# Kernel optimization log

Measured on AMD Instinct MI355X. Metric: run time of the kernel, lower is better.

## Reference

```python
import jax, jax.numpy as jnp
import numpy as np

F = 128   # flattened observation features
H = 64    # MLP/LSTM hidden size (hardcoded in module)
A = 15    # number of discrete actions
T = 128   # rollout length (timesteps)
B = 2048  # number of parallel envs (batch)


def setup_inputs() -> dict:
    key = jax.random.key(0)
    ks = jax.random.split(key, 12)
    n = lambda k, sh, s=1.0: jax.random.normal(k, sh, jnp.float32) * s
    return {
        "x": n(ks[0], (T * B, F)),
        "done": (jax.random.uniform(ks[1], (T * B,)) < 0.05).astype(jnp.float32),
        "h0": n(ks[2], (1, B, H)),
        "c0": n(ks[3], (1, B, H)),
        # MLP encoder params (Linear stores y = x @ W + b here, W: [in, out])
        "W1": n(ks[4], (F, H), 0.1), "b1": jnp.zeros((H,), jnp.float32),
        "W2": n(ks[5], (H, H), 0.1), "b2": jnp.zeros((H,), jnp.float32),
        # LSTM params, PyTorch layout: weight_ih [4H, H_in], gate order i,f,g,o
        "Wih": n(ks[6], (4 * H, H), 0.1), "bih": jnp.zeros((4 * H,), jnp.float32),
        "Whh": n(ks[7], (4 * H, H), 0.1), "bhh": jnp.zeros((4 * H,), jnp.float32),
        # actor / critic heads
        "Wa": n(ks[8], (H, A), 0.01), "ba": jnp.zeros((A,), jnp.float32),
        "Wc": n(ks[9], (H, 1), 1.0), "bc": jnp.zeros((1,), jnp.float32),
    }


def reference(x, done, h0, c0, W1, b1, W2, b2, Wih, bih, Whh, bhh, Wa, ba, Wc, bc):
    Bsz, Hh = h0.shape[1], h0.shape[2]
    # MLP encoder: Linear -> Tanh -> Linear -> Tanh
    y = jnp.tanh(x @ W1 + b1)
    y = jnp.tanh(y @ W2 + b2)                 # [T*B, H]
    y = y.reshape(-1, Bsz, Hh)                # [T, B, H]
    d = done.reshape(-1, Bsz)                 # [T, B]

    def step(carry, td):
        h, c = carry
        yt, dt = td
        m = (1.0 - dt)[:, None]               # done-mask hidden reset
        h = h * m
        c = c * m
        g = yt @ Wih.T + bih + h @ Whh.T + bhh  # [B, 4H]
        i, f, gg, o = jnp.split(g, 4, axis=-1)
        c = jax.nn.sigmoid(f) * c + jax.nn.sigmoid(i) * jnp.tanh(gg)
        h = jax.nn.sigmoid(o) * jnp.tanh(c)
        return (h, c), h

    (hT, cT), outs = jax.lax.scan(step, (h0[0], c0[0]), (y, d))
    z = outs.reshape(-1, Hh)                  # [T*B, H]
    logits = z @ Wa + ba                      # Categorical logits
    vf = z @ Wc + bc
    return logits, vf, hT[None], cT[None]
```

## Files before the change

### kernel.cpp

```cpp
#include <hip/hip_runtime.h>
#include <hip/hip_bf16.h>
#include <stdint.h>

typedef __bf16  bf16x8 __attribute__((ext_vector_type(8)));
typedef short   s16x8  __attribute__((ext_vector_type(8)));
typedef int     i32x4  __attribute__((ext_vector_type(4)));
typedef float   f32x4  __attribute__((ext_vector_type(4)));

union Frag { s16x8 s; bf16x8 b; i32x4 i; };

static __device__ __forceinline__ short f2bf(float f) {
    union { float f; unsigned u; } v; v.f = f;
    unsigned r = (v.u + 0x7FFFu + ((v.u >> 16) & 1u)) >> 16;
    return (short)r;
}
static __device__ __forceinline__ float bf2f(short s) {
    union { unsigned u; float f; } v; v.u = ((unsigned)(unsigned short)s) << 16;
    return v.f;
}
static __device__ __forceinline__ float fast_rcp(float x) { return __builtin_amdgcn_rcpf(x); }
static __device__ __forceinline__ float sigm(float x) { return fast_rcp(1.0f + __expf(-x)); }
static __device__ __forceinline__ float tanh_fast(float x) {
    float e = __expf(-2.0f * x);
    return (1.0f - e) * fast_rcp(1.0f + e);
}
static __device__ __forceinline__ f32x4 mfma16(bf16x8 a, bf16x8 b, f32x4 c) {
    return __builtin_amdgcn_mfma_f32_16x16x32_bf16(a, b, c, 0, 0, 0);
}

static __device__ __forceinline__ void block_sync_lds() {
    asm volatile("s_waitcnt lgkmcnt(0)\n\ts_barrier" ::: "memory");
}

#define GLDS(gp, lp) __builtin_amdgcn_global_load_lds( \
    (const __attribute__((address_space(1))) void*)(gp), \
    (__attribute__((address_space(3))) void*)(lp), 16, 0, 0)

#define TT 128
#define BB 2048
#define HH 64
#define FF 128
#define AA 15
#define CH 8
#define LOGITS_OFF 0
#define VF_OFF   3932160
#define HT_OFF   4194304
#define CT_OFF   4325376


__global__ __launch_bounds__(256) void enc_kernel(
    const float* __restrict__ x, const float* __restrict__ W1, const float* __restrict__ b1,
    const float* __restrict__ W2, const float* __restrict__ b2, short* __restrict__ y_sw)
{
    __shared__ short w1t[64][136];
    __shared__ short w2t[64][72];
    __shared__ short c1buf[4][16][72];
    __shared__ short ybuf[4][16][72];

    const int tid  = threadIdx.x;
    const int lane = tid & 63;
    const int w    = tid >> 6;
    const int c    = lane & 15;
    const int q    = lane >> 4;

    for (int i = tid; i < 128*64; i += 256) { int k = i >> 6, n = i & 63; w1t[n][k] = f2bf(W1[i]); }
    for (int i = tid; i < 64*64;  i += 256) { int k = i >> 6, n = i & 63; w2t[n][k] = f2bf(W2[i]); }

    float b1v[4], b2v[4];
#pragma unroll
    for (int ct = 0; ct < 4; ++ct) { b1v[ct] = b1[16*ct + c]; b2v[ct] = b2[16*ct + c]; }
    __syncthreads();

    for (int it = 0; it < 4; ++it) {
        const int wt = it*4096 + blockIdx.x*4 + w;
        const int r0 = wt * 16;
        Frag af[4];
#pragma unroll
        for (int kf = 0; kf < 4; ++kf) {
            const float* xp = x + (size_t)(r0 + c)*FF + 32*kf + 8*q;
            f32x4 x0 = *(const f32x4*)xp;
            f32x4 x1 = *(const f32x4*)(xp + 4);
#pragma unroll
            for (int jj = 0; jj < 4; ++jj) { af[kf].s[jj] = f2bf(x0[jj]); af[kf].s[4+jj] = f2bf(x1[jj]); }
        }
        f32x4 acc[4];
#pragma unroll
        for (int ct = 0; ct < 4; ++ct) acc[ct] = (f32x4){b1v[ct], b1v[ct], b1v[ct], b1v[ct]};
#pragma unroll
        for (int kf = 0; kf < 4; ++kf)
#pragma unroll
            for (int ct = 0; ct < 4; ++ct) {
                Frag bf; bf.s = *(const s16x8*)&w1t[16*ct + c][32*kf + 8*q];
                acc[ct] = mfma16(af[kf].b, bf.b, acc[ct]);
            }
#pragma unroll
        for (int ct = 0; ct < 4; ++ct)
#pragma unroll
            for (int i = 0; i < 4; ++i)
                c1buf[w][4*q + i][16*ct + c] = f2bf(tanh_fast(acc[ct][i]));
        Frag a2[2];
#pragma unroll
        for (int kf = 0; kf < 2; ++kf) a2[kf].s = *(const s16x8*)&c1buf[w][c][32*kf + 8*q];
        f32x4 acc2[4];
#pragma unroll
        for (int ct = 0; ct < 4; ++ct) acc2[ct] = (f32x4){b2v[ct], b2v[ct], b2v[ct], b2v[ct]};
#pragma unroll
        for (int kf = 0; kf < 2; ++kf)
#pragma unroll
            for (int ct = 0; ct < 4; ++ct) {
                Frag bf; bf.s = *(const s16x8*)&w2t[16*ct + c][32*kf + 8*q];
                acc2[ct] = mfma16(a2[kf].b, bf.b, acc2[ct]);
            }
#pragma unroll
        for (int ct = 0; ct < 4; ++ct)
#pragma unroll
            for (int i = 0; i < 4; ++i)
                ybuf[w][4*q + i][16*ct + c] = f2bf(tanh_fast(acc2[ct][i]));
        {
            const int kf2 = lane >> 5;
            const int c8  = (lane >> 2) & 7;
            const int qq  = lane & 3;
#pragma unroll
            for (int g = 0; g < 2; ++g) {
                s16x8 yv = *(const s16x8*)&ybuf[w][c8 + 8*g][32*kf2 + 8*qq];
                *(s16x8*)(y_sw + ((size_t)(wt >> 7)*256 + (size_t)(wt & 127)*2 + g)*512 + lane*8) = yv;
            }
        }
    }
}

__global__ __launch_bounds__(512, 1) void scan_kernel(
    const short* __restrict__ y_sw, const float* __restrict__ done,
    const float* __restrict__ h0, const float* __restrict__ c0,
    const float* __restrict__ Wih, const float* __restrict__ bih,
    const float* __restrict__ Whh, const float* __restrict__ bhh,
    const float* __restrict__ Wa, const float* __restrict__ ba,
    const float* __restrict__ Wc, const float* __restrict__ bc,
    float* __restrict__ out_logits, float* __restrict__ out_vf,
    float* __restrict__ hT_out, float* __restrict__ cT_out)
{
    __shared__ short ybuf[2][CH][512];
    __shared__ float gybuf[2][4][4][128];
    __shared__ float obuf[2][CH][8][16];
    __shared__ short zbuf[2][8][72];
    __shared__ short hbuf[2][8][72];
    __shared__ float dbuf[TT+1][8];

    const int tid  = threadIdx.x;
    const int lane = tid & 63;
    const int w    = tid >> 6;
    const int c    = lane & 15;
    const int q    = lane >> 4;
    const int blk  = blockIdx.x;
    const int b0   = blk * 8;
    const bool crit = (w < 4);
    const int hw   = w - 4;
    const int r0   = 4*(q & 1) + 2*(q >> 1);

    Frag  wf[4][2];
    float biasv[4];
    Frag  hwf[2];
    float hbv = 0.f;
    float cst0 = 0.f, cst1 = 0.f;

    if (crit) {
        const int jcol = 16*w + c;
#pragma unroll
        for (int a = 0; a < 4; ++a) {
            const int col = 64*a + jcol;
#pragma unroll
            for (int kf = 0; kf < 2; ++kf) {
                const float* wp = Whh + (size_t)col*HH + 32*kf + 8*q;
                f32x4 w0 = *(const f32x4*)wp;
                f32x4 w1 = *(const f32x4*)(wp + 4);
#pragma unroll
                for (int jj = 0; jj < 4; ++jj) { wf[a][kf].s[jj] = f2bf(w0[jj]); wf[a][kf].s[4+jj] = f2bf(w1[jj]); }
            }
        }
    } else {
        const int jcolh = 16*hw + c;
#pragma unroll
        for (int a = 0; a < 4; ++a) {
            const int col = 64*a + jcolh;
            biasv[a] = bih[col] + bhh[col];
#pragma unroll
            for (int kf = 0; kf < 2; ++kf) {
                const float* wp = Wih + (size_t)col*HH + 32*kf + 8*q;
                f32x4 w0 = *(const f32x4*)wp;
                f32x4 w1 = *(const f32x4*)(wp + 4);
#pragma unroll
                for (int jj = 0; jj < 4; ++jj) { wf[a][kf].s[jj] = f2bf(w0[jj]); wf[a][kf].s[4+jj] = f2bf(w1[jj]); }
            }
        }
#pragma unroll
        for (int kf = 0; kf < 2; ++kf)
#pragma unroll
            for (int jj = 0; jj < 8; ++jj) {
                int k = 32*kf + 8*q + jj;
                hwf[kf].s[jj] = f2bf((c < 15) ? Wa[k*AA + c] : Wc[k]);
            }
        hbv = (c < 15) ? ba[c] : bc[0];
        {
            const int t0 = hw * 32;
            const float* gp = done + (size_t)(t0 + (lane >> 1))*BB + b0 + 4*(lane & 1);
            GLDS(gp, &dbuf[t0][0]);
        }
#pragma unroll
        for (int i = 0; i < 2; ++i) {
            const int ss = hw*2 + i;
            const short* gp = y_sw + ((size_t)ss*256 + blk)*512 + lane*8;
            GLDS(gp, &ybuf[0][ss][0]);
        }
        __builtin_amdgcn_s_waitcnt(0x0F70);
    }
    if (tid < 8) dbuf[TT][tid] = 0.0f;
    __syncthreads();

    if (crit) {
        const int jcol = 16*w + c;
        {
            float d0 = dbuf[0][r0 + 0];
            float d1 = dbuf[0][r0 + 1];
            float cv0 = c0[(size_t)(b0 + r0 + 0)*HH + jcol];
            float cv1 = c0[(size_t)(b0 + r0 + 1)*HH + jcol];
            cst0 = (d0 != 0.0f) ? 0.0f : cv0;
            cst1 = (d1 != 0.0f) ? 0.0f : cv1;
        }
        if (tid < 128) {
            int mm = tid & 7, j4 = (tid >> 3) & 15;
            float dm = dbuf[0][mm];
            f32x4 hv = *(const f32x4*)(h0 + (size_t)(b0 + mm)*HH + 4*j4);
#pragma unroll
            for (int ii = 0; ii < 4; ++ii)
                hbuf[0][mm][4*j4 + ii] = (dm != 0.0f) ? (short)0 : f2bf(hv[ii]);
        }
    } else {
        Frag yc0, yc1;
        yc0.s = *(const s16x8*)&ybuf[0][0][((c & 7)*4 + q)*8];
        yc1.s = *(const s16x8*)&ybuf[0][0][(32 + (c & 7)*4 + q)*8];
#pragma unroll
        for (int a = 0; a < 4; ++a) {
            f32x4 gg = (f32x4){biasv[a], biasv[a], biasv[a], biasv[a]};
            gg = mfma16(yc0.b, wf[a][0].b, gg);
            gg = mfma16(yc1.b, wf[a][1].b, gg);
            if (lane < 32) *(f32x4*)&gybuf[0][hw][a][lane*4] = gg;
        }
    }
    __syncthreads();

    for (int t = 0; t < TT; ++t) {
        if (crit) {
            const int jcol = 16*w + c;
            const int cur = t & 1;
            Frag hf0, hf1;
            hf0.s = *(const s16x8*)&hbuf[cur][c & 7][8*q];
            hf1.s = *(const s16x8*)&hbuf[cur][c & 7][32 + 8*q];
            f32x4 acc[4];
#pragma unroll
            for (int a = 0; a < 4; ++a) acc[a] = *(const f32x4*)&gybuf[cur][w][a][(lane & 31)*4];
#pragma unroll
            for (int a = 0; a < 4; ++a) {
                acc[a] = mfma16(hf0.b, wf[a][0].b, acc[a]);
                acc[a] = mfma16(hf1.b, wf[a][1].b, acc[a]);
            }
            const int pidx = (lane ^ 32) << 2;
            float g0[4], g1[4];
            const bool hiq = (q >= 2);
#pragma unroll
            for (int a = 0; a < 4; ++a) {
                float s0 = __int_as_float(__builtin_amdgcn_ds_bpermute(pidx, __float_as_int(acc[a][2])));
                float s1 = __int_as_float(__builtin_amdgcn_ds_bpermute(pidx, __float_as_int(acc[a][3])));
                g0[a] = hiq ? s0 : acc[a][0];
                g1[a] = hiq ? s1 : acc[a][1];
            }
            const float dn0 = dbuf[t+1][r0 + 0];
            const float dn1 = dbuf[t+1][r0 + 1];
#define ELEM(GV, CSTV, RI, DN) {                                        \
            float ei = __expf(-GV[0]), ef = __expf(-GV[1]);             \
            float eg = __expf(-2.0f*GV[2]), eo = __expf(-GV[3]);        \
            float term = (1.0f - eg) * fast_rcp((1.0f + ei)*(1.0f + eg)); \
            float cn = fast_rcp(1.0f + ef)*CSTV + term;                 \
            float ec = __expf(-2.0f*cn);                                \
            float hv = (1.0f - ec) * fast_rcp((1.0f + eo)*(1.0f + ec)); \
            short zb = f2bf(hv);                                        \
            zbuf[cur][RI][jcol] = zb;                                   \
            const bool d = ((DN) != 0.0f);                              \
            CSTV = d ? 0.0f : cn;                                       \
            hbuf[cur ^ 1][RI][jcol] = d ? (short)0 : zb; }
            ELEM(g0, cst0, r0 + 0, dn0)
            ELEM(g1, cst1, r0 + 1, dn1)
#undef ELEM
        } else {
            if ((t & 7) == 0 && t < 120) {
                const int k = (t >> 3) + 1;
#pragma unroll
                for (int i = 0; i < 2; ++i) {
                    const int ss = hw*2 + i;
                    const short* gp = y_sw + ((size_t)(8*k + ss)*256 + blk)*512 + lane*8;
                    GLDS(gp, &ybuf[k & 1][ss][0]);
                }
            }
            if ((t & 7) == 1 && t > 8 && w == 4) {
                const int cc = (t >> 3) - 1;
                const int s = lane >> 3, r = lane & 7;
                const size_t row = (size_t)(8*cc + s)*BB + b0 + r;
                const float* ob = &obuf[cc & 1][s][r][0];
                float* lp = out_logits + row*AA;
#pragma unroll
                for (int n = 0; n < 15; ++n) lp[n] = ob[n];
                out_vf[row] = ob[15];
            }
            if (t >= 1 && w == 4 + ((t + 2) & 3)) {
                const int tp = t - 1;
                Frag zf0, zf1;
                zf0.s = *(const s16x8*)&zbuf[tp & 1][c & 7][8*q];
                zf1.s = *(const s16x8*)&zbuf[tp & 1][c & 7][32 + 8*q];
                f32x4 ha = (f32x4){hbv, hbv, hbv, hbv};
                ha = mfma16(zf0.b, hwf[0].b, ha);
                ha = mfma16(zf1.b, hwf[1].b, ha);
                if (q < 2) {
#pragma unroll
                    for (int i = 0; i < 4; ++i)
                        obuf[(tp >> 3) & 1][tp & 7][4*q + i][c] = ha[i];
                }
            }
            if (t < TT-1) {
                const int tn = t + 1;
                const int ch = (tn >> 3) & 1, sl = tn & 7;
                Frag yc0, yc1;
                yc0.s = *(const s16x8*)&ybuf[ch][sl][((c & 7)*4 + q)*8];
                yc1.s = *(const s16x8*)&ybuf[ch][sl][(32 + (c & 7)*4 + q)*8];
#pragma unroll
                for (int a = 0; a < 4; ++a) {
                    f32x4 g = (f32x4){biasv[a], biasv[a], biasv[a], biasv[a]};
                    g = mfma16(yc0.b, wf[a][0].b, g);
                    g = mfma16(yc1.b, wf[a][1].b, g);
                    if (lane < 32) *(f32x4*)&gybuf[tn & 1][hw][a][lane*4] = g;
                }
            }
            if ((t & 7) == 6)
                __builtin_amdgcn_s_waitcnt(0x0F70);
        }
        block_sync_lds();
    }

    if (!crit && w == 7) {
        Frag zf0, zf1;
        zf0.s = *(const s16x8*)&zbuf[1][c & 7][8*q];
        zf1.s = *(const s16x8*)&zbuf[1][c & 7][32 + 8*q];
        f32x4 ha = (f32x4){hbv, hbv, hbv, hbv};
        ha = mfma16(zf0.b, hwf[0].b, ha);
        ha = mfma16(zf1.b, hwf[1].b, ha);
        if (q < 2) {
#pragma unroll
            for (int i = 0; i < 4; ++i) obuf[1][7][4*q + i][c] = ha[i];
        }
    }
    __syncthreads();
    if (!crit && w == 4) {
        const int s = lane >> 3, r = lane & 7;
        const size_t row = (size_t)(120 + s)*BB + b0 + r;
        const float* ob = &obuf[1][s][r][0];
        float* lp = out_logits + row*AA;
#pragma unroll
        for (int n = 0; n < 15; ++n) lp[n] = ob[n];
        out_vf[row] = ob[15];
    }
    if (tid < 128) {
        int mm = tid & 7, j4 = (tid >> 3) & 15;
        f32x4 hv;
#pragma unroll
        for (int ii = 0; ii < 4; ++ii) hv[ii] = bf2f(zbuf[1][mm][4*j4 + ii]);
        *(f32x4*)(hT_out + (size_t)(b0 + mm)*HH + 4*j4) = hv;
    }
    if (crit) {
        const int jcol = 16*w + c;
        cT_out[(size_t)(b0 + r0 + 0)*HH + jcol] = cst0;
        cT_out[(size_t)(b0 + r0 + 1)*HH + jcol] = cst1;
    }
}

extern "C" void kernel_launch(void* const* d_in, const int* in_sizes, int n_in,
                              void* d_out, int out_size, void* d_ws, size_t ws_size,
                              hipStream_t stream) {
    const float* x    = (const float*)d_in[0];
    const float* done = (const float*)d_in[1];
    const float* h0   = (const float*)d_in[2];
    const float* c0   = (const float*)d_in[3];
    const float* W1   = (const float*)d_in[4];
    const float* b1   = (const float*)d_in[5];
    const float* W2   = (const float*)d_in[6];
    const float* b2   = (const float*)d_in[7];
    const float* Wih  = (const float*)d_in[8];
    const float* bih  = (const float*)d_in[9];
    const float* Whh  = (const float*)d_in[10];
    const float* bhh  = (const float*)d_in[11];
    const float* Wa   = (const float*)d_in[12];
    const float* ba   = (const float*)d_in[13];
    const float* Wc   = (const float*)d_in[14];
    const float* bc   = (const float*)d_in[15];
    float* out = (float*)d_out;

    short* y_sw = (short*)d_ws;

    enc_kernel<<<1024, 256, 0, stream>>>(x, W1, b1, W2, b2, y_sw);
    scan_kernel<<<256, 512, 0, stream>>>(y_sw, done, h0, c0, Wih, bih, Whh, bhh,
                                         Wa, ba, Wc, bc,
                                         out + LOGITS_OFF, out + VF_OFF,
                                         out + HT_OFF, out + CT_OFF);
}
```

Baseline: 310.2 us.

## Move input-gate MFMA into critical waves, keep gate preactivations in registers

Critical-path waves now hold both the Wih and Whh bf16 fragments. They compute the next step's input projection (y@Wih+bias) themselves, overlapped with the elementwise gate math, so the LDS gybuf staging buffer goes away. The lane-swap ds_bpermute is also replaced by a direct register select. That select only gives the same values if the accumulator layout of the fused y-projection lines up with what the bpermute used to fix. The cost is more registers and extra MFMA work inside the serial recurrence.

Result: faster. 295.0 us (-4.9%).

```diff
diff --git a/kernel.cpp b/kernel.cpp
--- a/kernel.cpp
+++ b/kernel.cpp
@@ -140,7 +140,6 @@
     float* __restrict__ hT_out, float* __restrict__ cT_out)
 {
     __shared__ short ybuf[2][CH][512];
-    __shared__ float gybuf[2][4][4][128];
     __shared__ float obuf[2][CH][8][16];
     __shared__ short zbuf[2][8][72];
     __shared__ short hbuf[2][8][72];
@@ -158,16 +157,19 @@
     const int r0   = 4*(q & 1) + 2*(q >> 1);
 
     Frag  wf[4][2];
+    Frag  wfi[4][2];
     float biasv[4];
     Frag  hwf[2];
     float hbv = 0.f;
     float cst0 = 0.f, cst1 = 0.f;
+    f32x4 gyr[4];
 
     if (crit) {
         const int jcol = 16*w + c;
 #pragma unroll
         for (int a = 0; a < 4; ++a) {
             const int col = 64*a + jcol;
+            biasv[a] = bih[col] + bhh[col];
 #pragma unroll
             for (int kf = 0; kf < 2; ++kf) {
                 const float* wp = Whh + (size_t)col*HH + 32*kf + 8*q;
@@ -175,23 +177,14 @@
                 f32x4 w1 = *(const f32x4*)(wp + 4);
 #pragma unroll
                 for (int jj = 0; jj < 4; ++jj) { wf[a][kf].s[jj] = f2bf(w0[jj]); wf[a][kf].s[4+jj] = f2bf(w1[jj]); }
+                const float* vp = Wih + (size_t)col*HH + 32*kf + 8*q;
+                f32x4 v0 = *(const f32x4*)vp;
+                f32x4 v1 = *(const f32x4*)(vp + 4);
+#pragma unroll
+                for (int jj = 0; jj < 4; ++jj) { wfi[a][kf].s[jj] = f2bf(v0[jj]); wfi[a][kf].s[4+jj] = f2bf(v1[jj]); }
             }
         }
     } else {
-        const int jcolh = 16*hw + c;
-#pragma unroll
-        for (int a = 0; a < 4; ++a) {
-            const int col = 64*a + jcolh;
-            biasv[a] = bih[col] + bhh[col];
-#pragma unroll
-            for (int kf = 0; kf < 2; ++kf) {
-                const float* wp = Wih + (size_t)col*HH + 32*kf + 8*q;
-                f32x4 w0 = *(const f32x4*)wp;
-                f32x4 w1 = *(const f32x4*)(wp + 4);
-#pragma unroll
-                for (int jj = 0; jj < 4; ++jj) { wf[a][kf].s[jj] = f2bf(w0[jj]); wf[a][kf].s[4+jj] = f2bf(w1[jj]); }
-            }
-        }
 #pragma unroll
         for (int kf = 0; kf < 2; ++kf)
 #pragma unroll
@@ -234,16 +227,17 @@
             for (int ii = 0; ii < 4; ++ii)
                 hbuf[0][mm][4*j4 + ii] = (dm != 0.0f) ? (short)0 : f2bf(hv[ii]);
         }
-    } else {
-        Frag yc0, yc1;
-        yc0.s = *(const s16x8*)&ybuf[0][0][((c & 7)*4 + q)*8];
-        yc1.s = *(const s16x8*)&ybuf[0][0][(32 + (c & 7)*4 + q)*8];
-#pragma unroll
-        for (int a = 0; a < 4; ++a) {
-            f32x4 gg = (f32x4){biasv[a], biasv[a], biasv[a], biasv[a]};
-            gg = mfma16(yc0.b, wf[a][0].b, gg);
-            gg = mfma16(yc1.b, wf[a][1].b, gg);
-            if (lane < 32) *(f32x4*)&gybuf[0][hw][a][lane*4] = gg;
+        {
+            Frag yc0, yc1;
+            yc0.s = *(const s16x8*)&ybuf[0][0][((c & 7)*4 + q)*8];
+            yc1.s = *(const s16x8*)&ybuf[0][0][(32 + (c & 7)*4 + q)*8];
+#pragma unroll
+            for (int a = 0; a < 4; ++a) {
+                f32x4 g = (f32x4){biasv[a], biasv[a], biasv[a], biasv[a]};
+                g = mfma16(yc0.b, wfi[a][0].b, g);
+                g = mfma16(yc1.b, wfi[a][1].b, g);
+                gyr[a] = g;
+            }
         }
     }
     __syncthreads();
@@ -257,24 +251,33 @@
             hf1.s = *(const s16x8*)&hbuf[cur][c & 7][32 + 8*q];
             f32x4 acc[4];
 #pragma unroll
-            for (int a = 0; a < 4; ++a) acc[a] = *(const f32x4*)&gybuf[cur][w][a][(lane & 31)*4];
-#pragma unroll
             for (int a = 0; a < 4; ++a) {
-                acc[a] = mfma16(hf0.b, wf[a][0].b, acc[a]);
+                acc[a] = mfma16(hf0.b, wf[a][0].b, gyr[a]);
                 acc[a] = mfma16(hf1.b, wf[a][1].b, acc[a]);
             }
-            const int pidx = (lane ^ 32) << 2;
+            const bool hiq = (q >= 2);
             float g0[4], g1[4];
-            const bool hiq = (q >= 2);
 #pragma unroll
             for (int a = 0; a < 4; ++a) {
-                float s0 = __int_as_float(__builtin_amdgcn_ds_bpermute(pidx, __float_as_int(acc[a][2])));
-                float s1 = __int_as_float(__builtin_amdgcn_ds_bpermute(pidx, __float_as_int(acc[a][3])));
-                g0[a] = hiq ? s0 : acc[a][0];
-                g1[a] = hiq ? s1 : acc[a][1];
+                g0[a] = hiq ? acc[a][2] : acc[a][0];
+                g1[a] = hiq ? acc[a][3] : acc[a][1];
             }
             const float dn0 = dbuf[t+1][r0 + 0];
             const float dn1 = dbuf[t+1][r0 + 1];
+            if (t < TT-1) {
+                const int tn = t + 1;
+                const int ch = (tn >> 3) & 1, sl = tn & 7;
+                Frag yc0, yc1;
+                yc0.s = *(const s16x8*)&ybuf[ch][sl][((c & 7)*4 + q)*8];
+                yc1.s = *(const s16x8*)&ybuf[ch][sl][(32 + (c & 7)*4 + q)*8];
+#pragma unroll
+                for (int a = 0; a < 4; ++a) {
+                    f32x4 g = (f32x4){biasv[a], biasv[a], biasv[a], biasv[a]};
+                    g = mfma16(yc0.b, wfi[a][0].b, g);
+                    g = mfma16(yc1.b, wfi[a][1].b, g);
+                    gyr[a] = g;
+                }
+            }
 #define ELEM(GV, CSTV, RI, DN) {                                        \
             float ei = __expf(-GV[0]), ef = __expf(-GV[1]);             \
             float eg = __expf(-2.0f*GV[2]), eo = __expf(-GV[3]);        \
@@ -322,20 +325,6 @@
 #pragma unroll
                     for (int i = 0; i < 4; ++i)
                         obuf[(tp >> 3) & 1][tp & 7][4*q + i][c] = ha[i];
-                }
-            }
-            if (t < TT-1) {
-                const int tn = t + 1;
-                const int ch = (tn >> 3) & 1, sl = tn & 7;
-                Frag yc0, yc1;
-                yc0.s = *(const s16x8*)&ybuf[ch][sl][((c & 7)*4 + q)*8];
-                yc1.s = *(const s16x8*)&ybuf[ch][sl][(32 + (c & 7)*4 + q)*8];
-#pragma unroll
-                for (int a = 0; a < 4; ++a) {
-                    f32x4 g = (f32x4){biasv[a], biasv[a], biasv[a], biasv[a]};
-                    g = mfma16(yc0.b, wf[a][0].b, g);
-                    g = mfma16(yc1.b, wf[a][1].b, g);
-                    if (lane < 32) *(f32x4*)&gybuf[tn & 1][hw][a][lane*4] = g;
                 }
             }
             if ((t & 7) == 6)
```
